# Performance work log

Measured on AMD Instinct MI355X. Metric: run time of the kernel, lower is better.

The kernel has to match this reference:

```python
import jax, jax.numpy as jnp
import numpy as np

N_QUBITS = 8
DIM = 2 ** N_QUBITS  # 256
BSZ = 32768
N_OPS = 20

# Deterministic stand-in for tq.RandomLayer(n_ops=20): a fixed random list of
# {rx, ry, rz, cnot} ops on random wires, angles supplied via rl_angles.
_rng = np.random.RandomState(0)
_RL_OPS = []
for _i in range(N_OPS):
    _kind = ['rx', 'ry', 'rz', 'cnot'][int(_rng.randint(4))]
    if _kind == 'cnot':
        _w = _rng.choice(N_QUBITS, 2, replace=False)
        _RL_OPS.append((_kind, int(_w[0]), int(_w[1])))
    else:
        _RL_OPS.append((_kind, int(_rng.randint(N_QUBITS)), -1))


def _apply_1q(state, wire, kind, half_angle):
    """Apply a single-qubit rotation to state [bsz, DIM]. wire 0 = MSB."""
    bsz = state.shape[0]
    left = 2 ** wire
    right = DIM // (2 * left)
    st = state.reshape(bsz, left, 2, right)
    ha = jnp.broadcast_to(jnp.asarray(half_angle).reshape(-1), (bsz,))
    c = jnp.cos(ha)[:, None, None]
    s = jnp.sin(ha)[:, None, None]
    s0, s1 = st[:, :, 0, :], st[:, :, 1, :]
    if kind == 'ry':
        n0, n1 = c * s0 - s * s1, s * s0 + c * s1
    elif kind == 'rx':
        n0, n1 = c * s0 - 1j * s * s1, -1j * s * s0 + c * s1
    else:  # rz
        n0, n1 = (c - 1j * s) * s0, (c + 1j * s) * s1
    return jnp.stack([n0, n1], axis=2).reshape(bsz, DIM)


def _apply_cnot(state, control, target):
    bsz = state.shape[0]
    st = state.reshape((bsz,) + (2,) * N_QUBITS)
    c_ax, t_ax = 1 + control, 1 + target
    a = jnp.take(st, 0, axis=c_ax)  # control = 0 block: identity
    b = jnp.take(st, 1, axis=c_ax)  # control = 1 block: X on target
    b = jnp.flip(b, axis=t_ax - (1 if t_ax > c_ax else 0))
    return jnp.stack([a, b], axis=c_ax).reshape(bsz, DIM)


# Precomputed PauliZ sign table: signs[w, k] = +1 if bit w of k is 0 else -1.
_idx = np.arange(DIM)
_bits = (_idx[None, :] >> (N_QUBITS - 1 - np.arange(N_QUBITS)[:, None])) & 1
_SIGNS = jnp.asarray(1.0 - 2.0 * _bits, jnp.float32)  # [N_QUBITS, DIM]


def setup_inputs() -> dict:
    key = jax.random.key(0)
    k1, k2, k3, k4 = jax.random.split(key, 4)
    return {
        'x': jax.random.uniform(k1, (BSZ, N_QUBITS), dtype=jnp.float32),
        'rl_angles': jax.random.normal(k2, (N_OPS,), dtype=jnp.float32),
        'theta_rx': jax.random.normal(k3, (1,), dtype=jnp.float32),
        'theta_ry': jax.random.normal(k4, (1,), dtype=jnp.float32),
    }


def reference(x, rl_angles, theta_rx, theta_ry):
    bsz = x.shape[0]
    # |0...0> initial state
    state = jnp.zeros((bsz, DIM), jnp.complex64).at[:, 0].set(1.0)
    # GeneralEncoder: RY(x_i) on wire i (per-sample angles)
    for i in range(N_QUBITS):
        state = _apply_1q(state, i, 'ry', x[:, i] * 0.5)
    # RandomLayer: 20 fixed random ops
    for k, (kind, w0, w1) in enumerate(_RL_OPS):
        if kind == 'cnot':
            state = _apply_cnot(state, w0, w1)
        else:
            state = _apply_1q(state, w0, kind, rl_angles[k] * 0.5)
    # shared trainable RX then RY on every wire
    for w in range(N_QUBITS):
        state = _apply_1q(state, w, 'rx', theta_rx[0] * 0.5)
        state = _apply_1q(state, w, 'ry', theta_ry[0] * 0.5)
    # MeasureAll(PauliZ): <Z_w> = sum_k |amp_k|^2 * sign(bit_w(k))
    probs = state.real ** 2 + state.imag ** 2  # [bsz, DIM]
    return probs @ _SIGNS.T  # [bsz, N_QUBITS]
```

## Files before the change

kernel.cpp:

```cpp
#include <hip/hip_runtime.h>
#include <stdint.h>

#define NQ 8
#define DIM 256
#define BSZ 32768
#define NOPS 20

typedef float v2f __attribute__((ext_vector_type(2)));


struct COps { int kind[NOPS]; int w0[NOPS]; int w1[NOPS]; };

struct CMT {
  uint32_t mt[624]; int pos;
  constexpr CMT(uint32_t seed) : mt{}, pos(624) {
    for (int i = 0; i < 624; ++i) {
      mt[i] = seed;
      seed = 1812433253u * (seed ^ (seed >> 30)) + (uint32_t)(i + 1);
    }
  }
  constexpr uint32_t next32() {
    if (pos >= 624) {
      for (int i = 0; i < 624; ++i) {
        uint32_t y = (mt[i] & 0x80000000u) | (mt[(i + 1) % 624] & 0x7fffffffu);
        mt[i] = mt[(i + 397) % 624] ^ (y >> 1) ^ ((y & 1u) ? 0x9908b0dfu : 0u);
      }
      pos = 0;
    }
    uint32_t y = mt[pos++];
    y ^= y >> 11; y ^= (y << 7) & 0x9d2c5680u; y ^= (y << 15) & 0xefc60000u; y ^= y >> 18;
    return y;
  }
  constexpr uint32_t interval(uint32_t mx) {
    if (mx == 0u) return 0u;
    uint32_t mask = mx;
    mask |= mask >> 1; mask |= mask >> 2; mask |= mask >> 4; mask |= mask >> 8; mask |= mask >> 16;
    uint32_t v = next32() & mask;
    while (v > mx) v = next32() & mask;
    return v;
  }
};

constexpr COps decode_ops() {
  COps o{}; CMT r(0u);
  for (int k = 0; k < NOPS; ++k) {
    const uint32_t kind = r.interval(3u);
    o.kind[k] = (int)kind;
    if (kind == 3u) {
      int perm[NQ] = {0,1,2,3,4,5,6,7};
      for (int i = NQ - 1; i >= 1; --i) {
        const uint32_t j = r.interval((uint32_t)i);
        const int t = perm[i]; perm[i] = perm[(int)j]; perm[(int)j] = t;
      }
      o.w0[k] = perm[0]; o.w1[k] = perm[1];
    } else {
      o.w0[k] = (int)r.interval(7u);
      o.w1[k] = -1;
    }
  }
  return o;
}

constexpr COps OPS = decode_ops();


template<int MASK>
__device__ __forceinline__ float lanexf(float v) {
  int i = __builtin_bit_cast(int, v);
  int r;
  if constexpr (MASK == 1)      r = __builtin_amdgcn_update_dpp(0, i, 0xB1, 0xF, 0xF, true);
  else if constexpr (MASK == 2) r = __builtin_amdgcn_update_dpp(0, i, 0x4E, 0xF, 0xF, true);
  else if constexpr (MASK == 8) r = __builtin_amdgcn_update_dpp(0, i, 0x128, 0xF, 0xF, true);
  else                          r = __builtin_amdgcn_ds_swizzle(i, 0x101F);
  return __builtin_bit_cast(float, r);
}

template<int MASK>
__device__ __forceinline__ v2f lanex2(v2f v) {
  v2f r; r.x = lanexf<MASK>(v.x); r.y = lanexf<MASK>(v.y); return r;
}

__device__ __forceinline__ v2f vswap(v2f v) { return __builtin_shufflevector(v, v, 1, 0); }
__device__ __forceinline__ v2f vsplat(float s) { v2f r = {s, s}; return r; }


template<int W>
__device__ __forceinline__ void g_rx_t(v2f (&v)[16], int l, float t) {
  constexpr int m = 1 << (7 - W);
  const v2f tpm = {t, -t};
  if constexpr (m >= 16) {
    constexpr int M = m >> 4;
    #pragma unroll
    for (int j0 = 0; j0 < 16; ++j0) if ((j0 & M) == 0) {
      const int j1 = j0 | M;
      v2f a = v[j0], b = v[j1];
      v[j0] = a + tpm * vswap(b);
      v[j1] = b + tpm * vswap(a);
    }
  } else {
    #pragma unroll
    for (int j = 0; j < 16; ++j) {
      v2f x = lanex2<m>(v[j]);
      v[j] = v[j] + tpm * vswap(x);
    }
  }
}

template<int W>
__device__ __forceinline__ void g_ry_t(v2f (&v)[16], int l, float t) {
  constexpr int m = 1 << (7 - W);
  if constexpr (m >= 16) {
    constexpr int M = m >> 4;
    const v2f vtn = vsplat(-t), vtp = vsplat(t);
    #pragma unroll
    for (int j0 = 0; j0 < 16; ++j0) if ((j0 & M) == 0) {
      const int j1 = j0 | M;
      v2f a = v[j0], b = v[j1];
      v[j0] = a + vtn * b;
      v[j1] = b + vtp * a;
    }
  } else {
    const v2f ts = vsplat((l & m) ? t : -t);
    #pragma unroll
    for (int j = 0; j < 16; ++j) {
      v2f x = lanex2<m>(v[j]);
      v[j] = v[j] + ts * x;
    }
  }
}

template<int W>
__device__ __forceinline__ void g_rz_t(v2f (&v)[16], int l, float t) {
  constexpr int m = 1 << (7 - W);
  if constexpr (m >= 16) {
    constexpr int M = m >> 4;
    const v2f tpm = {t, -t};
    #pragma unroll
    for (int j = 0; j < 16; ++j) {
      v2f sw = vswap(v[j]);
      if ((j & M) == 0) v[j] = v[j] + tpm * sw;
      else              v[j] = v[j] - tpm * sw;
    }
  } else {
    const v2f ts = (l & m) ? (v2f){-t, t} : (v2f){t, -t};
    #pragma unroll
    for (int j = 0; j < 16; ++j) v[j] = v[j] + ts * vswap(v[j]);
  }
}

template<int WC, int WT>
__device__ __forceinline__ void g_cnot(v2f (&v)[16], int l) {
  constexpr int mc = 1 << (7 - WC);
  constexpr int mt = 1 << (7 - WT);
  if constexpr (mt >= 16) {
    constexpr int M = mt >> 4;
    if constexpr (mc >= 16) {
      constexpr int MC = mc >> 4;
      #pragma unroll
      for (int j0 = 0; j0 < 16; ++j0) if ((j0 & M) == 0 && (j0 & MC) != 0) {
        const int j1 = j0 | M;
        v2f t = v[j0]; v[j0] = v[j1]; v[j1] = t;
      }
    } else {
      const bool bit = (l & mc) != 0;
      #pragma unroll
      for (int j0 = 0; j0 < 16; ++j0) if ((j0 & M) == 0) {
        const int j1 = j0 | M;
        v2f a = v[j0], b = v[j1];
        v[j0] = bit ? b : a;
        v[j1] = bit ? a : b;
      }
    }
  } else {
    if constexpr (mc >= 16) {
      constexpr int MC = mc >> 4;
      #pragma unroll
      for (int j = 0; j < 16; ++j) if (j & MC) v[j] = lanex2<mt>(v[j]);
    } else if constexpr ((mc == 8 || mc == 4) && mt != 4) {
      constexpr int BM   = (mc == 8) ? 0xC : 0xA;
      constexpr int ctrl = (mt == 1) ? 0xB1 : (mt == 2) ? 0x4E : 0x128;
      #pragma unroll
      for (int j = 0; j < 16; ++j) {
        int ir = __builtin_bit_cast(int, v[j].x);
        int ii = __builtin_bit_cast(int, v[j].y);
        ir = __builtin_amdgcn_update_dpp(ir, ir, ctrl, 0xF, BM, false);
        ii = __builtin_amdgcn_update_dpp(ii, ii, ctrl, 0xF, BM, false);
        v[j].x = __builtin_bit_cast(float, ir);
        v[j].y = __builtin_bit_cast(float, ii);
      }
    } else {
      const bool bit = (l & mc) != 0;
      #pragma unroll
      for (int j = 0; j < 16; ++j) {
        v2f x = lanex2<mt>(v[j]);
        v[j] = bit ? x : v[j];
      }
    }
  }
}

template<int K>
__device__ __forceinline__ void apply_ops(v2f (&v)[16], int l, const float* __restrict__ rl, float& cacc) {
  if constexpr (K < NOPS) {
    constexpr int kind = OPS.kind[K];
    if constexpr (kind == 3) {
      g_cnot<OPS.w0[K], OPS.w1[K]>(v, l);
    } else {
      float sn, cs;
      __sincosf(0.5f * rl[K], &sn, &cs);
      const float t = sn * __builtin_amdgcn_rcpf(cs);
      cacc *= cs;
      if constexpr      (kind == 0) g_rx_t<OPS.w0[K]>(v, l, t);
      else if constexpr (kind == 1) g_ry_t<OPS.w0[K]>(v, l, t);
      else                          g_rz_t<OPS.w0[K]>(v, l, t);
    }
    apply_ops<K + 1>(v, l, rl, cacc);
  }
}


template<int M>
__device__ __forceinline__ float xy_inlane(const v2f (&v)[16], float tnx, float tny) {
  v2f aRe = {0.f, 0.f}, aIm = {0.f, 0.f};
  #pragma unroll
  for (int j0 = 0; j0 < 16; ++j0) if ((j0 & M) == 0) {
    const int j1 = j0 | M;
    aRe += v[j0] * v[j1];
    aIm += v[j0] * vswap(v[j1]);
  }
  return tnx * (aRe.x + aRe.y) + tny * (aIm.x - aIm.y);
}

template<int MASK>
__device__ __forceinline__ float xy_cross(const v2f (&v)[16], int l, float nx, float ny) {
  v2f aRe = {0.f, 0.f}, aIm = {0.f, 0.f};
  #pragma unroll
  for (int j = 0; j < 16; ++j) {
    v2f x = lanex2<MASK>(v[j]);
    aRe += v[j] * x;
    aIm += v[j] * vswap(x);
  }
  const float nys = (l & MASK) ? -ny : ny;
  return nx * (aRe.x + aRe.y) + nys * (aIm.x - aIm.y);
}

__global__ __launch_bounds__(256)
void qcnn_kernel(const float* __restrict__ x, const float* __restrict__ rl,
                 const float* __restrict__ thx, const float* __restrict__ thy,
                 float* __restrict__ out)
{
  const int tid = blockIdx.x * blockDim.x + threadIdx.x;
  const int b = tid >> 4;
  const int l = tid & 15;

  const float4* xp = reinterpret_cast<const float4*>(x + (size_t)b * 8);
  const float4 xa = xp[0], xb = xp[1];
  float sw[8], cw[8];
  __sincosf(0.5f * xa.x, &sw[0], &cw[0]);
  __sincosf(0.5f * xa.y, &sw[1], &cw[1]);
  __sincosf(0.5f * xa.z, &sw[2], &cw[2]);
  __sincosf(0.5f * xa.w, &sw[3], &cw[3]);
  __sincosf(0.5f * xb.x, &sw[4], &cw[4]);
  __sincosf(0.5f * xb.y, &sw[5], &cw[5]);
  __sincosf(0.5f * xb.z, &sw[6], &cw[6]);
  __sincosf(0.5f * xb.w, &sw[7], &cw[7]);

  const float pl = ((l & 8) ? sw[4] : cw[4]) * ((l & 4) ? sw[5] : cw[5]) *
                   ((l & 2) ? sw[6] : cw[6]) * ((l & 1) ? sw[7] : cw[7]);
  const float p01[4] = {cw[0]*cw[1], cw[0]*sw[1], sw[0]*cw[1], sw[0]*sw[1]};
  const float p23[4] = {cw[2]*cw[3], cw[2]*sw[3], sw[2]*cw[3], sw[2]*sw[3]};
  const float p01l[4] = {p01[0]*pl, p01[1]*pl, p01[2]*pl, p01[3]*pl};

  v2f v[16];
  #pragma unroll
  for (int j = 0; j < 16; ++j) { v[j].x = p01l[j >> 2] * p23[j & 3]; v[j].y = 0.f; }

  float cacc = 1.0f;
  apply_ops<0>(v, l, rl, cacc);
  const float C2 = cacc * cacc;

  float sxf, cxf, syf, cyf;
  __sincosf(thx[0], &sxf, &cxf);
  __sincosf(thy[0], &syf, &cyf);
  const float nx = -syf * C2, ny = cyf * sxf * C2, nz = cyf * cxf * C2;
  const float tnx = 2.f * nx, tny = 2.f * ny;

  v2f P2 = {0,0}, A0v = {0,0}, A1v = {0,0}, A2v = {0,0}, A3v = {0,0};
  #pragma unroll
  for (int j = 0; j < 16; ++j) {
    const v2f q = v[j] * v[j];
    P2 += q;
    if (j & 8) A0v -= q; else A0v += q;
    if (j & 4) A1v -= q; else A1v += q;
    if (j & 2) A2v -= q; else A2v += q;
    if (j & 1) A3v -= q; else A3v += q;
  }
  const float P  = P2.x + P2.y;
  const float A0 = A0v.x + A0v.y, A1 = A1v.x + A1v.y;
  const float A2 = A2v.x + A2v.y, A3 = A3v.x + A3v.y;

  float t0 = fmaf(nz, A0, xy_inlane<8>(v, tnx, tny));
  float t1 = fmaf(nz, A1, xy_inlane<4>(v, tnx, tny));
  float t2 = fmaf(nz, A2, xy_inlane<2>(v, tnx, tny));
  float t3 = fmaf(nz, A3, xy_inlane<1>(v, tnx, tny));
  float t4 = fmaf(nz, (l & 8) ? -P : P, xy_cross<8>(v, l, nx, ny));
  float t5 = fmaf(nz, (l & 4) ? -P : P, xy_cross<4>(v, l, nx, ny));
  float t6 = fmaf(nz, (l & 2) ? -P : P, xy_cross<2>(v, l, nx, ny));
  float t7 = fmaf(nz, (l & 1) ? -P : P, xy_cross<1>(v, l, nx, ny));

  #define RED_STEP(MK) \
    t0 += lanexf<MK>(t0); t1 += lanexf<MK>(t1); t2 += lanexf<MK>(t2); t3 += lanexf<MK>(t3); \
    t4 += lanexf<MK>(t4); t5 += lanexf<MK>(t5); t6 += lanexf<MK>(t6); t7 += lanexf<MK>(t7);
  RED_STEP(1) RED_STEP(2) RED_STEP(4) RED_STEP(8)
  #undef RED_STEP

  if (l == 0) {
    float4* o = reinterpret_cast<float4*>(out + (size_t)b * 8);
    const float4 o0 = {t0, t1, t2, t3};
    const float4 o1 = {t4, t5, t6, t7};
    o[0] = o0; o[1] = o1;
  }
}


extern "C" void kernel_launch(void* const* d_in, const int* in_sizes, int n_in,
                              void* d_out, int out_size, void* d_ws, size_t ws_size,
                              hipStream_t stream) {
  const float* x   = (const float*)d_in[0];
  const float* rl  = (const float*)d_in[1];
  const float* thx = (const float*)d_in[2];
  const float* thy = (const float*)d_in[3];
  float* out = (float*)d_out;

  const int threads = 256;
  const int blocks = BSZ / (threads / 16);
  qcnn_kernel<<<blocks, threads, 0, stream>>>(x, rl, thx, thy, out);
}
```

Baseline: 24.02 us.

## Process two samples per thread group and replace swizzle with DPP pair

Each 16-lane group now simulates two batch samples at once, interleaving their gate applications. The goal is more instruction-level parallelism to hide DPP and ALU latency, and the shared per-op sincos is computed once for both samples. The grid is halved and register pressure roughly doubles, which may lower occupancy. The xor-4 lane exchange now uses two DPP ops (half-mirror then quad reverse) instead of ds_swizzle, avoiding the LDS-path instruction.

Result: slower. 27.95 us (+16.4%).

```diff
diff --git a/kernel.cpp b/kernel.cpp
--- a/kernel.cpp
+++ b/kernel.cpp
@@ -71,7 +71,10 @@
   if constexpr (MASK == 1)      r = __builtin_amdgcn_update_dpp(0, i, 0xB1, 0xF, 0xF, true);
   else if constexpr (MASK == 2) r = __builtin_amdgcn_update_dpp(0, i, 0x4E, 0xF, 0xF, true);
   else if constexpr (MASK == 8) r = __builtin_amdgcn_update_dpp(0, i, 0x128, 0xF, 0xF, true);
-  else                          r = __builtin_amdgcn_ds_swizzle(i, 0x101F);
+  else {
+    int h = __builtin_amdgcn_update_dpp(0, i, 0x141, 0xF, 0xF, true);
+    r     = __builtin_amdgcn_update_dpp(0, h, 0x1B, 0xF, 0xF, true);
+  }
   return __builtin_bit_cast(float, r);
 }
 
@@ -200,19 +203,20 @@
 }
 
 template<int K>
-__device__ __forceinline__ void apply_ops(v2f (&v)[16], int l, const float* __restrict__ rl, float& cacc) {
+__device__ __forceinline__ void apply_ops(v2f (&v)[2][16], int l, const float* __restrict__ rl, float& cacc) {
   if constexpr (K < NOPS) {
     constexpr int kind = OPS.kind[K];
     if constexpr (kind == 3) {
-      g_cnot<OPS.w0[K], OPS.w1[K]>(v, l);
+      g_cnot<OPS.w0[K], OPS.w1[K]>(v[0], l);
+      g_cnot<OPS.w0[K], OPS.w1[K]>(v[1], l);
     } else {
       float sn, cs;
       __sincosf(0.5f * rl[K], &sn, &cs);
       const float t = sn * __builtin_amdgcn_rcpf(cs);
       cacc *= cs;
-      if constexpr      (kind == 0) g_rx_t<OPS.w0[K]>(v, l, t);
-      else if constexpr (kind == 1) g_ry_t<OPS.w0[K]>(v, l, t);
-      else                          g_rz_t<OPS.w0[K]>(v, l, t);
+      if constexpr      (kind == 0) { g_rx_t<OPS.w0[K]>(v[0], l, t); g_rx_t<OPS.w0[K]>(v[1], l, t); }
+      else if constexpr (kind == 1) { g_ry_t<OPS.w0[K]>(v[0], l, t); g_ry_t<OPS.w0[K]>(v[1], l, t); }
+      else                          { g_rz_t<OPS.w0[K]>(v[0], l, t); g_rz_t<OPS.w0[K]>(v[1], l, t); }
     }
     apply_ops<K + 1>(v, l, rl, cacc);
   }
@@ -244,16 +248,8 @@
   return nx * (aRe.x + aRe.y) + nys * (aIm.x - aIm.y);
 }
 
-__global__ __launch_bounds__(256)
-void qcnn_kernel(const float* __restrict__ x, const float* __restrict__ rl,
-                 const float* __restrict__ thx, const float* __restrict__ thy,
-                 float* __restrict__ out)
-{
-  const int tid = blockIdx.x * blockDim.x + threadIdx.x;
-  const int b = tid >> 4;
-  const int l = tid & 15;
-
-  const float4* xp = reinterpret_cast<const float4*>(x + (size_t)b * 8);
+__device__ __forceinline__ void init_state(v2f (&v)[16], const float* __restrict__ xrow, int l) {
+  const float4* xp = reinterpret_cast<const float4*>(xrow);
   const float4 xa = xp[0], xb = xp[1];
   float sw[8], cw[8];
   __sincosf(0.5f * xa.x, &sw[0], &cw[0]);
@@ -270,10 +266,23 @@
   const float p01[4] = {cw[0]*cw[1], cw[0]*sw[1], sw[0]*cw[1], sw[0]*sw[1]};
   const float p23[4] = {cw[2]*cw[3], cw[2]*sw[3], sw[2]*cw[3], sw[2]*sw[3]};
   const float p01l[4] = {p01[0]*pl, p01[1]*pl, p01[2]*pl, p01[3]*pl};
-
-  v2f v[16];
   #pragma unroll
   for (int j = 0; j < 16; ++j) { v[j].x = p01l[j >> 2] * p23[j & 3]; v[j].y = 0.f; }
+}
+
+__global__ __launch_bounds__(256)
+void qcnn_kernel(const float* __restrict__ x, const float* __restrict__ rl,
+                 const float* __restrict__ thx, const float* __restrict__ thy,
+                 float* __restrict__ out)
+{
+  const int tid = blockIdx.x * blockDim.x + threadIdx.x;
+  const int p = tid >> 4;
+  const int l = tid & 15;
+  const int b0 = 2 * p;
+
+  v2f v[2][16];
+  init_state(v[0], x + (size_t)b0 * 8, l);
+  init_state(v[1], x + (size_t)(b0 + 1) * 8, l);
 
   float cacc = 1.0f;
   apply_ops<0>(v, l, rl, cacc);
@@ -285,39 +294,48 @@
   const float nx = -syf * C2, ny = cyf * sxf * C2, nz = cyf * cxf * C2;
   const float tnx = 2.f * nx, tny = 2.f * ny;
 
-  v2f P2 = {0,0}, A0v = {0,0}, A1v = {0,0}, A2v = {0,0}, A3v = {0,0};
-  #pragma unroll
-  for (int j = 0; j < 16; ++j) {
-    const v2f q = v[j] * v[j];
-    P2 += q;
-    if (j & 8) A0v -= q; else A0v += q;
-    if (j & 4) A1v -= q; else A1v += q;
-    if (j & 2) A2v -= q; else A2v += q;
-    if (j & 1) A3v -= q; else A3v += q;
-  }
-  const float P  = P2.x + P2.y;
-  const float A0 = A0v.x + A0v.y, A1 = A1v.x + A1v.y;
-  const float A2 = A2v.x + A2v.y, A3 = A3v.x + A3v.y;
-
-  float t0 = fmaf(nz, A0, xy_inlane<8>(v, tnx, tny));
-  float t1 = fmaf(nz, A1, xy_inlane<4>(v, tnx, tny));
-  float t2 = fmaf(nz, A2, xy_inlane<2>(v, tnx, tny));
-  float t3 = fmaf(nz, A3, xy_inlane<1>(v, tnx, tny));
-  float t4 = fmaf(nz, (l & 8) ? -P : P, xy_cross<8>(v, l, nx, ny));
-  float t5 = fmaf(nz, (l & 4) ? -P : P, xy_cross<4>(v, l, nx, ny));
-  float t6 = fmaf(nz, (l & 2) ? -P : P, xy_cross<2>(v, l, nx, ny));
-  float t7 = fmaf(nz, (l & 1) ? -P : P, xy_cross<1>(v, l, nx, ny));
-
-  #define RED_STEP(MK) \
-    t0 += lanexf<MK>(t0); t1 += lanexf<MK>(t1); t2 += lanexf<MK>(t2); t3 += lanexf<MK>(t3); \
-    t4 += lanexf<MK>(t4); t5 += lanexf<MK>(t5); t6 += lanexf<MK>(t6); t7 += lanexf<MK>(t7);
-  RED_STEP(1) RED_STEP(2) RED_STEP(4) RED_STEP(8)
-  #undef RED_STEP
-
-  if (l == 0) {
-    float4* o = reinterpret_cast<float4*>(out + (size_t)b * 8);
-    const float4 o0 = {t0, t1, t2, t3};
-    const float4 o1 = {t4, t5, t6, t7};
+  float t[2][8];
+  #pragma unroll
+  for (int s = 0; s < 2; ++s) {
+    v2f P2 = {0,0}, A0v = {0,0}, A1v = {0,0}, A2v = {0,0}, A3v = {0,0};
+    #pragma unroll
+    for (int j = 0; j < 16; ++j) {
+      const v2f q = v[s][j] * v[s][j];
+      P2 += q;
+      if (j & 8) A0v -= q; else A0v += q;
+      if (j & 4) A1v -= q; else A1v += q;
+      if (j & 2) A2v -= q; else A2v += q;
+      if (j & 1) A3v -= q; else A3v += q;
+    }
+    const float P  = P2.x + P2.y;
+    const float A0 = A0v.x + A0v.y, A1 = A1v.x + A1v.y;
+    const float A2 = A2v.x + A2v.y, A3 = A3v.x + A3v.y;
+
+    t[s][0] = fmaf(nz, A0, xy_inlane<8>(v[s], tnx, tny));
+    t[s][1] = fmaf(nz, A1, xy_inlane<4>(v[s], tnx, tny));
+    t[s][2] = fmaf(nz, A2, xy_inlane<2>(v[s], tnx, tny));
+    t[s][3] = fmaf(nz, A3, xy_inlane<1>(v[s], tnx, tny));
+    t[s][4] = fmaf(nz, (l & 8) ? -P : P, xy_cross<8>(v[s], l, nx, ny));
+    t[s][5] = fmaf(nz, (l & 4) ? -P : P, xy_cross<4>(v[s], l, nx, ny));
+    t[s][6] = fmaf(nz, (l & 2) ? -P : P, xy_cross<2>(v[s], l, nx, ny));
+    t[s][7] = fmaf(nz, (l & 1) ? -P : P, xy_cross<1>(v[s], l, nx, ny));
+  }
+
+  #pragma unroll
+  for (int s = 0; s < 2; ++s) {
+    #pragma unroll
+    for (int q = 0; q < 8; ++q) {
+      t[s][q] += lanexf<1>(t[s][q]);
+      t[s][q] += lanexf<2>(t[s][q]);
+      t[s][q] += lanexf<4>(t[s][q]);
+      t[s][q] += lanexf<8>(t[s][q]);
+    }
+  }
+
+  if (l < 2) {
+    float4* o = reinterpret_cast<float4*>(out + (size_t)(b0 + l) * 8);
+    const float4 o0 = {t[l][0], t[l][1], t[l][2], t[l][3]};
+    const float4 o1 = {t[l][4], t[l][5], t[l][6], t[l][7]};
     o[0] = o0; o[1] = o1;
   }
 }
@@ -333,6 +351,6 @@
   float* out = (float*)d_out;
 
   const int threads = 256;
-  const int blocks = BSZ / (threads / 16);
+  const int blocks = BSZ / (2 * (threads / 16));
   qcnn_kernel<<<blocks, threads, 0, stream>>>(x, rl, thx, thy, out);
 }
```

## Process two samples per thread group and hoist rotation-parameter math out of loop

Applied to the files above, without the earlier changes.

Each 16-lane group now simulates two batch samples in a loop, so the per-op sincos/rcp for the 20 random-layer angles and the final trainable-rotation constants are computed once per thread and reused. The tangent values are made wave-uniform with readfirstlane so they can live in scalar registers. The lane-xor-4 exchange switches from ds_swizzle to two DPP row operations. In exchange the grid is halved, which reduces parallelism and latency hiding, and the tv array adds register pressure.

Measured after the change: 25.67 us. +6.9%, slower.

```diff
diff --git a/kernel.cpp b/kernel.cpp
--- a/kernel.cpp
+++ b/kernel.cpp
@@ -5,6 +5,7 @@
 #define DIM 256
 #define BSZ 32768
 #define NOPS 20
+#define SPT 2
 
 typedef float v2f __attribute__((ext_vector_type(2)));
 
@@ -64,6 +65,10 @@
 constexpr COps OPS = decode_ops();
 
 
+__device__ __forceinline__ float rfl(float v) {
+  return __builtin_bit_cast(float, __builtin_amdgcn_readfirstlane(__builtin_bit_cast(int, v)));
+}
+
 template<int MASK>
 __device__ __forceinline__ float lanexf(float v) {
   int i = __builtin_bit_cast(int, v);
@@ -71,7 +76,10 @@
   if constexpr (MASK == 1)      r = __builtin_amdgcn_update_dpp(0, i, 0xB1, 0xF, 0xF, true);
   else if constexpr (MASK == 2) r = __builtin_amdgcn_update_dpp(0, i, 0x4E, 0xF, 0xF, true);
   else if constexpr (MASK == 8) r = __builtin_amdgcn_update_dpp(0, i, 0x128, 0xF, 0xF, true);
-  else                          r = __builtin_amdgcn_ds_swizzle(i, 0x101F);
+  else {
+    int h = __builtin_amdgcn_update_dpp(0, i, 0x141, 0xF, 0xF, true);
+    r     = __builtin_amdgcn_update_dpp(0, h, 0x1B, 0xF, 0xF, true);
+  }
   return __builtin_bit_cast(float, r);
 }
 
@@ -200,21 +208,27 @@
 }
 
 template<int K>
-__device__ __forceinline__ void apply_ops(v2f (&v)[16], int l, const float* __restrict__ rl, float& cacc) {
+__device__ __forceinline__ void compute_t(const float* __restrict__ rl, float (&tv)[NOPS], float& cacc) {
+  if constexpr (K < NOPS) {
+    if constexpr (OPS.kind[K] != 3) {
+      float sn, cs;
+      __sincosf(0.5f * rl[K], &sn, &cs);
+      tv[K] = rfl(sn * __builtin_amdgcn_rcpf(cs));
+      cacc *= cs;
+    }
+    compute_t<K + 1>(rl, tv, cacc);
+  }
+}
+
+template<int K>
+__device__ __forceinline__ void apply_ops(v2f (&v)[16], int l, const float (&tv)[NOPS]) {
   if constexpr (K < NOPS) {
     constexpr int kind = OPS.kind[K];
-    if constexpr (kind == 3) {
-      g_cnot<OPS.w0[K], OPS.w1[K]>(v, l);
-    } else {
-      float sn, cs;
-      __sincosf(0.5f * rl[K], &sn, &cs);
-      const float t = sn * __builtin_amdgcn_rcpf(cs);
-      cacc *= cs;
-      if constexpr      (kind == 0) g_rx_t<OPS.w0[K]>(v, l, t);
-      else if constexpr (kind == 1) g_ry_t<OPS.w0[K]>(v, l, t);
-      else                          g_rz_t<OPS.w0[K]>(v, l, t);
-    }
-    apply_ops<K + 1>(v, l, rl, cacc);
+    if constexpr (kind == 3)      g_cnot<OPS.w0[K], OPS.w1[K]>(v, l);
+    else if constexpr (kind == 0) g_rx_t<OPS.w0[K]>(v, l, tv[K]);
+    else if constexpr (kind == 1) g_ry_t<OPS.w0[K]>(v, l, tv[K]);
+    else                          g_rz_t<OPS.w0[K]>(v, l, tv[K]);
+    apply_ops<K + 1>(v, l, tv);
   }
 }
 
@@ -244,16 +258,8 @@
   return nx * (aRe.x + aRe.y) + nys * (aIm.x - aIm.y);
 }
 
-__global__ __launch_bounds__(256)
-void qcnn_kernel(const float* __restrict__ x, const float* __restrict__ rl,
-                 const float* __restrict__ thx, const float* __restrict__ thy,
-                 float* __restrict__ out)
-{
-  const int tid = blockIdx.x * blockDim.x + threadIdx.x;
-  const int b = tid >> 4;
-  const int l = tid & 15;
-
-  const float4* xp = reinterpret_cast<const float4*>(x + (size_t)b * 8);
+__device__ __forceinline__ void init_state(v2f (&v)[16], const float* __restrict__ xrow, int l) {
+  const float4* xp = reinterpret_cast<const float4*>(xrow);
   const float4 xa = xp[0], xb = xp[1];
   float sw[8], cw[8];
   __sincosf(0.5f * xa.x, &sw[0], &cw[0]);
@@ -270,13 +276,22 @@
   const float p01[4] = {cw[0]*cw[1], cw[0]*sw[1], sw[0]*cw[1], sw[0]*sw[1]};
   const float p23[4] = {cw[2]*cw[3], cw[2]*sw[3], sw[2]*cw[3], sw[2]*sw[3]};
   const float p01l[4] = {p01[0]*pl, p01[1]*pl, p01[2]*pl, p01[3]*pl};
-
-  v2f v[16];
   #pragma unroll
   for (int j = 0; j < 16; ++j) { v[j].x = p01l[j >> 2] * p23[j & 3]; v[j].y = 0.f; }
-
+}
+
+__global__ __launch_bounds__(256)
+void qcnn_kernel(const float* __restrict__ x, const float* __restrict__ rl,
+                 const float* __restrict__ thx, const float* __restrict__ thy,
+                 float* __restrict__ out)
+{
+  const int tid = blockIdx.x * blockDim.x + threadIdx.x;
+  const int p = tid >> 4;
+  const int l = tid & 15;
+
+  float tv[NOPS];
   float cacc = 1.0f;
-  apply_ops<0>(v, l, rl, cacc);
+  compute_t<0>(rl, tv, cacc);
   const float C2 = cacc * cacc;
 
   float sxf, cxf, syf, cyf;
@@ -285,40 +300,49 @@
   const float nx = -syf * C2, ny = cyf * sxf * C2, nz = cyf * cxf * C2;
   const float tnx = 2.f * nx, tny = 2.f * ny;
 
-  v2f P2 = {0,0}, A0v = {0,0}, A1v = {0,0}, A2v = {0,0}, A3v = {0,0};
-  #pragma unroll
-  for (int j = 0; j < 16; ++j) {
-    const v2f q = v[j] * v[j];
-    P2 += q;
-    if (j & 8) A0v -= q; else A0v += q;
-    if (j & 4) A1v -= q; else A1v += q;
-    if (j & 2) A2v -= q; else A2v += q;
-    if (j & 1) A3v -= q; else A3v += q;
-  }
-  const float P  = P2.x + P2.y;
-  const float A0 = A0v.x + A0v.y, A1 = A1v.x + A1v.y;
-  const float A2 = A2v.x + A2v.y, A3 = A3v.x + A3v.y;
-
-  float t0 = fmaf(nz, A0, xy_inlane<8>(v, tnx, tny));
-  float t1 = fmaf(nz, A1, xy_inlane<4>(v, tnx, tny));
-  float t2 = fmaf(nz, A2, xy_inlane<2>(v, tnx, tny));
-  float t3 = fmaf(nz, A3, xy_inlane<1>(v, tnx, tny));
-  float t4 = fmaf(nz, (l & 8) ? -P : P, xy_cross<8>(v, l, nx, ny));
-  float t5 = fmaf(nz, (l & 4) ? -P : P, xy_cross<4>(v, l, nx, ny));
-  float t6 = fmaf(nz, (l & 2) ? -P : P, xy_cross<2>(v, l, nx, ny));
-  float t7 = fmaf(nz, (l & 1) ? -P : P, xy_cross<1>(v, l, nx, ny));
-
-  #define RED_STEP(MK) \
-    t0 += lanexf<MK>(t0); t1 += lanexf<MK>(t1); t2 += lanexf<MK>(t2); t3 += lanexf<MK>(t3); \
-    t4 += lanexf<MK>(t4); t5 += lanexf<MK>(t5); t6 += lanexf<MK>(t6); t7 += lanexf<MK>(t7);
-  RED_STEP(1) RED_STEP(2) RED_STEP(4) RED_STEP(8)
-  #undef RED_STEP
-
-  if (l == 0) {
-    float4* o = reinterpret_cast<float4*>(out + (size_t)b * 8);
-    const float4 o0 = {t0, t1, t2, t3};
-    const float4 o1 = {t4, t5, t6, t7};
-    o[0] = o0; o[1] = o1;
+  #pragma unroll 1
+  for (int it = 0; it < SPT; ++it) {
+    const int b = p * SPT + it;
+
+    v2f v[16];
+    init_state(v, x + (size_t)b * 8, l);
+    apply_ops<0>(v, l, tv);
+
+    v2f P2 = {0,0}, A0v = {0,0}, A1v = {0,0}, A2v = {0,0}, A3v = {0,0};
+    #pragma unroll
+    for (int j = 0; j < 16; ++j) {
+      const v2f q = v[j] * v[j];
+      P2 += q;
+      if (j & 8) A0v -= q; else A0v += q;
+      if (j & 4) A1v -= q; else A1v += q;
+      if (j & 2) A2v -= q; else A2v += q;
+      if (j & 1) A3v -= q; else A3v += q;
+    }
+    const float P  = P2.x + P2.y;
+    const float A0 = A0v.x + A0v.y, A1 = A1v.x + A1v.y;
+    const float A2 = A2v.x + A2v.y, A3 = A3v.x + A3v.y;
+
+    float t0 = fmaf(nz, A0, xy_inlane<8>(v, tnx, tny));
+    float t1 = fmaf(nz, A1, xy_inlane<4>(v, tnx, tny));
+    float t2 = fmaf(nz, A2, xy_inlane<2>(v, tnx, tny));
+    float t3 = fmaf(nz, A3, xy_inlane<1>(v, tnx, tny));
+    float t4 = fmaf(nz, (l & 8) ? -P : P, xy_cross<8>(v, l, nx, ny));
+    float t5 = fmaf(nz, (l & 4) ? -P : P, xy_cross<4>(v, l, nx, ny));
+    float t6 = fmaf(nz, (l & 2) ? -P : P, xy_cross<2>(v, l, nx, ny));
+    float t7 = fmaf(nz, (l & 1) ? -P : P, xy_cross<1>(v, l, nx, ny));
+
+    #define RED_STEP(MK) \
+      t0 += lanexf<MK>(t0); t1 += lanexf<MK>(t1); t2 += lanexf<MK>(t2); t3 += lanexf<MK>(t3); \
+      t4 += lanexf<MK>(t4); t5 += lanexf<MK>(t5); t6 += lanexf<MK>(t6); t7 += lanexf<MK>(t7);
+    RED_STEP(1) RED_STEP(2) RED_STEP(4) RED_STEP(8)
+    #undef RED_STEP
+
+    if (l == 0) {
+      float4* o = reinterpret_cast<float4*>(out + (size_t)b * 8);
+      const float4 o0 = {t0, t1, t2, t3};
+      const float4 o1 = {t4, t5, t6, t7};
+      o[0] = o0; o[1] = o1;
+    }
   }
 }
 
@@ -333,6 +357,6 @@
   float* out = (float*)d_out;
 
   const int threads = 256;
-  const int blocks = BSZ / (threads / 16);
+  const int blocks = BSZ / (SPT * (threads / 16));
   qcnn_kernel<<<blocks, threads, 0, stream>>>(x, rl, thx, thy, out);
 }
```
